# Optimization experiments

Hardware: AMD Instinct MI355X
Metric: run time of the kernel (lower is better)

The kernel has to match this reference:

```python
import jax
import jax.numpy as jnp
import numpy as np


def setup_inputs() -> dict:
    key = jax.random.key(0)
    k1, k2 = jax.random.split(key)
    B, C, H, W = 2, 256, 64, 128  # 1/8-res RAFT features of a 512x1024 image
    fmap1 = jax.random.normal(k1, (B, C, H, W), dtype=jnp.float32)
    fmap2 = jax.random.normal(k2, (B, C, H, W), dtype=jnp.float32)
    return {"fmap1": fmap1, "fmap2": fmap2, "k": 32}


def reference(fmap1, fmap2, k):
    B, C, H, W = fmap1.shape
    N = H * W
    f1 = fmap1.reshape(B, C, N)
    f2 = fmap2.reshape(B, C, N)

    # --- KNN (FAISS inner-product search), indices are non-differentiable ---
    scores = jnp.einsum('bcn,bcm->bnm', jax.lax.stop_gradient(f1),
                        jax.lax.stop_gradient(f2))  # [B, N1, N2]
    _, idx = jax.lax.top_k(scores, k)               # [B, N1, k]
    idx = jnp.transpose(idx, (0, 2, 1))             # [B, k, N1]

    # --- gather top-k target features: gathered[b,c,j,n] = f2[b,c,idx[b,j,n]] ---
    gathered = jax.vmap(lambda f, i: f[:, i])(f2, idx)  # [B, C, k, N1]

    # --- sparse correlation ---
    corr_sp = jnp.einsum('bcn,bckn->bkn', f1, gathered) / jnp.sqrt(jnp.float32(C))

    # --- coordinate grids (y-first), relative displacement ---
    ys, xs = jnp.meshgrid(jnp.arange(H, dtype=jnp.float32),
                          jnp.arange(W, dtype=jnp.float32), indexing='ij')
    coords = jnp.stack([ys.ravel(), xs.ravel()])          # [2, N], y first
    coords0 = jnp.broadcast_to(coords[None, :, None, :], (B, 2, k, N))
    coords1 = jnp.transpose(coords[:, idx], (1, 0, 2, 3))  # [B, 2, k, N]
    coords1 = coords1 - coords0                            # relative offsets

    batch_index = jnp.broadcast_to(
        jnp.arange(B, dtype=jnp.float32).reshape(B, 1, 1, 1), (B, 1, k, N))

    return corr_sp, coords0, coords1, batch_index
```

## Files before the change

### kernel.cpp

```cpp
#include <hip/hip_runtime.h>
#include <hip/hip_bf16.h>

#define B_  2
#define C_  256
#define H_  64
#define W_  128
#define N_  (H_ * W_)
#define K_  32
#define Q_  16
#define CK2 36
#define TN  32
#define TM  32
#define NHT 64
#define RR  16

typedef short  short8  __attribute__((ext_vector_type(8)));
typedef short  short4v __attribute__((ext_vector_type(4)));
typedef float  floatx4 __attribute__((ext_vector_type(4)));

__device__ __forceinline__ unsigned umin_(unsigned a, unsigned b) { return a < b ? a : b; }
__device__ __forceinline__ unsigned umax_(unsigned a, unsigned b) { return a > b ? a : b; }
__device__ __forceinline__ ushort f2bf(float v) {
    __hip_bfloat16 h = __float2bfloat16(v);
    ushort u; __builtin_memcpy(&u, &h, 2); return u;
}
__device__ __forceinline__ unsigned med3u(unsigned a, unsigned b, unsigned c) {
    unsigned d;
    asm("v_med3_u32 %0, %1, %2, %3" : "=v"(d) : "v"(a), "v"(b), "v"(c));
    return d;
}

__device__ __forceinline__ unsigned packkey(float v, int m) {
    const float vc = v > 0.0f ? v : 0.0f;
    unsigned b; __builtin_memcpy(&b, &vc, 4);
    return (b & 0xFFFFE000u) | (unsigned)m;
}

__device__ __forceinline__ void qinsert(unsigned (&q)[Q_], unsigned k) {
#pragma unroll
    for (int i = Q_ - 1; i > 0; --i)
        q[i] = med3u(q[i - 1], k, q[i]);
    q[0] = umax_(q[0], k);
}

#define CSWAP(a, b) { const unsigned _mx = umax_(a, b); \
                      const unsigned _mn = umin_(a, b); (a) = _mx; (b) = _mn; }

__device__ __forceinline__ void bar_lgkm() {
    asm volatile("s_waitcnt lgkmcnt(0)" ::: "memory");
    __builtin_amdgcn_sched_barrier(0);
    __builtin_amdgcn_s_barrier();
    __builtin_amdgcn_sched_barrier(0);
}

__global__ void raft_prep_kernel(const float* __restrict__ f1,
                                 const float* __restrict__ f2,
                                 float* __restrict__ f1Tf,
                                 ushort* __restrict__ f2T,
                                 float* __restrict__ f2Tf) {
    __shared__ float tile[32][33];
    const int nt = blockIdx.x;
    const int ct = blockIdx.y;
    const int z  = blockIdx.z;
    const int b  = z >> 1;
    const float* __restrict__ src = (z & 1) ? f2 : f1;
    const int tid = threadIdx.x;

    {
        const int cl = tid >> 3;
        const int nx = tid & 7;
        const float4 v = *(const float4*)(
            src + ((size_t)b * C_ + (ct * 32 + cl)) * N_ + (nt * 32 + nx * 4));
        tile[cl][nx * 4 + 0] = v.x;
        tile[cl][nx * 4 + 1] = v.y;
        tile[cl][nx * 4 + 2] = v.z;
        tile[cl][nx * 4 + 3] = v.w;
    }
    __syncthreads();
    {
        const int nl = tid >> 3;
        const int c4 = (tid & 7) * 4;
        float4 v;
        v.x = tile[c4 + 0][nl];
        v.y = tile[c4 + 1][nl];
        v.z = tile[c4 + 2][nl];
        v.w = tile[c4 + 3][nl];
        const size_t o = ((size_t)b * N_ + (nt * 32 + nl)) * C_ + (ct * 32 + c4);
        if (z & 1) {
            *(float4*)(f2Tf + o) = v;
            short4v h;
            h[0] = (short)f2bf(v.x); h[1] = (short)f2bf(v.y);
            h[2] = (short)f2bf(v.z); h[3] = (short)f2bf(v.w);
            *(short4v*)(f2T + o) = h;
        } else {
            *(float4*)(f1Tf + o) = v;
        }
    }
}

__launch_bounds__(512, 4)
__global__ void raft_stage1_kernel(const float* __restrict__ f1Tf,
                                   const ushort* __restrict__ f2T,
                                   ushort* __restrict__ cand) {
    __shared__ __align__(16) ushort Bt[4][TM * 256];

    const int bid0 = blockIdx.x;
    const int bid  = ((bid0 & 7) << 6) | (bid0 >> 3);
    const int b    = bid >> 8;
    const int nt0  = (bid & 255) * TN;
    const int tid  = threadIdx.x;
    const int w    = tid >> 6;
    const int s    = w & 1;
    const int h    = w >> 1;
    const int lane = tid & 63;
    const int p    = lane & 15;
    const int q4   = lane >> 4;
    const int nrow = nt0 + s * 16 + p;
    const int mbase = h * (N_ / 4);
    const int lt   = tid & 127;

    short8 af[8];
    {
        const float* __restrict__ arow = f1Tf + ((size_t)b * N_ + nrow) * C_;
        #pragma unroll
        for (int ks = 0; ks < 8; ++ks) {
            const float4 x = *(const float4*)(arow + ks * 32 + q4 * 8);
            const float4 y = *(const float4*)(arow + ks * 32 + q4 * 8 + 4);
            short8 t;
            t[0] = (short)f2bf(x.x); t[1] = (short)f2bf(x.y);
            t[2] = (short)f2bf(x.z); t[3] = (short)f2bf(x.w);
            t[4] = (short)f2bf(y.x); t[5] = (short)f2bf(y.y);
            t[6] = (short)f2bf(y.z); t[7] = (short)f2bf(y.w);
            af[ks] = t;
        }
    }

    unsigned q[Q_];
    #pragma unroll
    for (int i = 0; i < Q_; ++i) q[i] = 0u;

    const ushort* __restrict__ Bb = f2T + (size_t)b * N_ * C_ + (size_t)mbase * C_;

    short8 stg[8];
    #pragma unroll
    for (int i = 0; i < 8; ++i) {
        const int idx = lt + 128 * i;
        const int r   = idx >> 5;
        const int c8  = idx & 31;
        stg[i] = *(const short8*)(Bb + (size_t)r * C_ + c8 * 8);
    }

    for (int mt = 0; mt < NHT; ++mt) {
        {
            ushort* __restrict__ dst = Bt[h];
            #pragma unroll
            for (int i = 0; i < 8; ++i) {
                const int idx = lt + 128 * i;
                const int r   = idx >> 5;
                const int c8  = idx & 31;
                *(short8*)(&dst[(r * 32 + (c8 ^ (r & 7))) * 8]) = stg[i];
            }
        }

        if (mt < NHT - 1) {
            const ushort* __restrict__ src = Bb + (size_t)(mt + 1) * TM * C_;
            #pragma unroll
            for (int i = 0; i < 8; ++i) {
                const int idx = lt + 128 * i;
                const int r   = idx >> 5;
                const int c8  = idx & 31;
                stg[i] = *(const short8*)(src + (size_t)r * C_ + c8 * 8);
            }
        }
        bar_lgkm();

        const ushort* __restrict__ cur = Bt[h];
        floatx4 acc[2];
        #pragma unroll
        for (int f = 0; f < 2; ++f) acc[f] = (floatx4){0.f, 0.f, 0.f, 0.f};
        #pragma unroll
        for (int ks = 0; ks < 8; ++ks) {
            #pragma unroll
            for (int f = 0; f < 2; ++f) {
                const short8 bm = *(const short8*)(
                    &cur[((f * 16 + p) * 32 + ((ks * 4 + q4) ^ (p & 7))) * 8]);
                acc[f] = __builtin_amdgcn_mfma_f32_16x16x32_bf16(bm, af[ks], acc[f], 0, 0, 0);
            }
        }

        const int m0 = mbase + mt * TM;
        #pragma unroll
        for (int f = 0; f < 2; ++f) {
            const int mb = m0 + f * 16 + q4 * 4;
            unsigned k0 = packkey(acc[f][0], mb + 0);
            unsigned k1 = packkey(acc[f][1], mb + 1);
            unsigned k2 = packkey(acc[f][2], mb + 2);
            unsigned k3 = packkey(acc[f][3], mb + 3);
            CSWAP(k0, k1); CSWAP(k2, k3); CSWAP(k0, k2); CSWAP(k1, k3); CSWAP(k1, k2);
            qinsert(q, k0);
            if (__any(k1 > q[Q_ - 1])) {
                qinsert(q, k1);
                if (__any(k2 > q[Q_ - 1])) {
                    qinsert(q, k2);
                    if (__any(k3 > q[Q_ - 1])) qinsert(q, k3);
                }
            }
        }
        bar_lgkm();
    }

    unsigned* __restrict__ mg = (unsigned*)&Bt[0][0];
    const int rowl = s * 16 + p;
    const int qi   = h * 4 + q4;
    #pragma unroll
    for (int t = 0; t < Q_; ++t)
        mg[(qi * Q_ + t) * 33 + rowl] = q[t];
    __syncthreads();

    unsigned* __restrict__ ms = mg + 8448;
    if (tid < 128) {
        const int r = tid >> 2, g = tid & 3;
        const unsigned* __restrict__ Lb = &mg[(g * 4) * Q_ * 33];
        unsigned* __restrict__ O = &ms[(g * CK2) * 33 + r];
        int i0 = 0, i1 = 0, i2 = 0, i3 = 0;
        for (int t = 0; t < CK2; ++t) {
            const unsigned a0 = (i0 < Q_) ? Lb[(0 * Q_ + i0) * 33 + r] : 0u;
            const unsigned a1 = (i1 < Q_) ? Lb[(1 * Q_ + i1) * 33 + r] : 0u;
            const unsigned a2 = (i2 < Q_) ? Lb[(2 * Q_ + i2) * 33 + r] : 0u;
            const unsigned a3 = (i3 < Q_) ? Lb[(3 * Q_ + i3) * 33 + r] : 0u;
            const unsigned m01 = umax_(a0, a1), m23 = umax_(a2, a3);
            const unsigned mx  = umax_(m01, m23);
            O[t * 33] = mx;
            i0 += (a0 == mx);
            i1 += (a0 != mx) & (a1 == mx);
            i2 += (a0 != mx) & (a1 != mx) & (a2 == mx);
            i3 += (a0 != mx) & (a1 != mx) & (a2 != mx) & (a3 == mx);
        }
    }
    __syncthreads();

    if (tid < 32) {
        int i0 = 0, i1 = 0, i2 = 0, i3 = 0;
        ushort* __restrict__ myc = cand + ((size_t)(b * N_ + nt0 + tid)) * CK2;
        for (int t = 0; t < CK2; ++t) {
            const unsigned a0 = ms[(0 * CK2 + i0) * 33 + tid];
            const unsigned a1 = ms[(1 * CK2 + i1) * 33 + tid];
            const unsigned a2 = ms[(2 * CK2 + i2) * 33 + tid];
            const unsigned a3 = ms[(3 * CK2 + i3) * 33 + tid];
            const unsigned m01 = umax_(a0, a1), m23 = umax_(a2, a3);
            const unsigned mx  = umax_(m01, m23);
            myc[t] = (ushort)(mx & 0x1FFFu);
            i0 += (a0 == mx);
            i1 += (a0 != mx) & (a1 == mx);
            i2 += (a0 != mx) & (a1 != mx) & (a2 == mx);
            i3 += (a0 != mx) & (a1 != mx) & (a2 != mx) & (a3 == mx);
        }
    }
}

__launch_bounds__(576)
__global__ void raft_rerank_kernel(const float* __restrict__ f1Tf,
                                   const float* __restrict__ f2Tf,
                                   const ushort* __restrict__ cand,
                                   float* __restrict__ out) {
    __shared__ float  aS[RR][C_];
    __shared__ float  cs[RR][CK2];
    __shared__ ushort cmS[RR][CK2];
    const int bid0 = blockIdx.x;
    const int bid  = ((bid0 & 7) << 7) | (bid0 >> 3);
    const int row0 = bid * RR;
    const int tid  = threadIdx.x;
    const int r    = tid / CK2;
    const int c    = tid - r * CK2;

    for (int sidx = tid; sidx < RR * (C_ / 4); sidx += RR * CK2) {
        const int rr = sidx >> 6, s4 = sidx & 63;
        const int rg = row0 + rr;
        const int bb = rg >> 13, nn = rg & (N_ - 1);
        *(float4*)(&aS[rr][s4 * 4]) =
            *(const float4*)(f1Tf + ((size_t)bb * N_ + nn) * C_ + s4 * 4);
    }
    cmS[r][c] = cand[(size_t)(row0 + r) * CK2 + c];
    __syncthreads();

    {
        const int rg = row0 + r;
        const int bb = rg >> 13;
        const int m  = cmS[r][c];
        const float* __restrict__ bRow = f2Tf + ((size_t)bb * N_ + m) * C_;
        float acc = 0.0f;
        for (int c4 = 0; c4 < C_; c4 += 4) {
            const float4 b4 = *(const float4*)(bRow + c4);
            acc = fmaf(aS[r][c4 + 0], b4.x, acc);
            acc = fmaf(aS[r][c4 + 1], b4.y, acc);
            acc = fmaf(aS[r][c4 + 2], b4.z, acc);
            acc = fmaf(aS[r][c4 + 3], b4.w, acc);
        }
        cs[r][c] = acc;
    }
    __syncthreads();

    const int rg = row0 + r;
    const int bb = rg >> 13;
    const int n  = rg & (N_ - 1);
    const int y0 = n >> 7, x0 = n & 127;
    {
        const float v = cs[r][c];
        const int m = cmS[r][c];
        int rank = 0;
        for (int j = 0; j < CK2; ++j) {
            const float vj = cs[r][j];
            rank += (vj > v) || ((vj == v) && (cmS[r][j] < m));
        }
        if (rank < K_) {
            const size_t posn = (size_t)rank * N_ + n;
            out[(size_t)bb * (K_ * N_) + posn] = v * 0.0625f;
            const size_t c1b = (size_t)1572864 + (size_t)bb * 2 * K_ * N_;
            out[c1b + posn]                     = (float)((m >> 7) - y0);
            out[c1b + (size_t)(K_ * N_) + posn] = (float)((m & 127) - x0);
        }
    }
    if (c < K_) {
        const size_t posn = (size_t)c * N_ + n;
        const size_t c0b = (size_t)524288 + (size_t)bb * 2 * K_ * N_;
        out[c0b + posn]                     = (float)y0;
        out[c0b + (size_t)(K_ * N_) + posn] = (float)x0;
        out[(size_t)2621440 + (size_t)bb * (K_ * N_) + posn] = (float)bb;
    }
}

extern "C" void kernel_launch(void* const* d_in, const int* in_sizes, int n_in,
                              void* d_out, int out_size, void* d_ws, size_t ws_size,
                              hipStream_t stream) {
    const float* f1 = (const float*)d_in[0];
    const float* f2 = (const float*)d_in[1];

    float*  f1Tf = (float*)d_ws;
    float*  f2Tf = f1Tf + (size_t)B_ * N_ * C_;
    ushort* f2T  = (ushort*)(f2Tf + (size_t)B_ * N_ * C_);
    ushort* cand = f2T + (size_t)B_ * N_ * C_;

    raft_prep_kernel<<<dim3(N_ / 32, C_ / 32, B_ * 2), dim3(256), 0, stream>>>(
        f1, f2, f1Tf, f2T, f2Tf);

    raft_stage1_kernel<<<dim3(B_ * (N_ / TN)), dim3(512), 0, stream>>>(f1Tf, f2T, cand);

    raft_rerank_kernel<<<dim3(B_ * N_ / RR), dim3(RR * CK2), 0, stream>>>(
        f1Tf, f2Tf, cand, (float*)d_out);
}
```

Measured before the change: 347.9 us.

## Load B fragments directly to registers, drop LDS staging and barriers in stage1

The stage-1 KNN kernel no longer stages f2 tiles through shared memory with per-tile barriers. Each wave now streams its own 16-row B fragments straight from global memory into registers, prefetching the next tile during the MFMA work. Each wave covers both 16-row query halves with two accumulators and two per-lane queues, and the queue depth drops from 16 to 10. The merge stage becomes an 8-way merge to match the changed split. This removes LDS writes and barrier stalls but raises register pressure (occupancy hint lowered to 2), increases global/L2 traffic with no LDS reuse, and the shallower per-lane queues risk losing true top-k candidates.

```diff
diff --git a/kernel.cpp b/kernel.cpp
--- a/kernel.cpp
+++ b/kernel.cpp
@@ -7,10 +7,10 @@
 #define W_  128
 #define N_  (H_ * W_)
 #define K_  32
-#define Q_  16
+#define Q_  10
 #define CK2 36
 #define TN  32
-#define TM  32
+#define TM  16
 #define NHT 64
 #define RR  16
 
@@ -45,13 +45,6 @@
 
 #define CSWAP(a, b) { const unsigned _mx = umax_(a, b); \
                       const unsigned _mn = umin_(a, b); (a) = _mx; (b) = _mn; }
-
-__device__ __forceinline__ void bar_lgkm() {
-    asm volatile("s_waitcnt lgkmcnt(0)" ::: "memory");
-    __builtin_amdgcn_sched_barrier(0);
-    __builtin_amdgcn_s_barrier();
-    __builtin_amdgcn_sched_barrier(0);
-}
 
 __global__ void raft_prep_kernel(const float* __restrict__ f1,
                                  const float* __restrict__ f2,
@@ -98,30 +91,27 @@
     }
 }
 
-__launch_bounds__(512, 4)
+__launch_bounds__(512, 2)
 __global__ void raft_stage1_kernel(const float* __restrict__ f1Tf,
                                    const ushort* __restrict__ f2T,
                                    ushort* __restrict__ cand) {
-    __shared__ __align__(16) ushort Bt[4][TM * 256];
+    __shared__ unsigned smem[15840];
 
     const int bid0 = blockIdx.x;
     const int bid  = ((bid0 & 7) << 6) | (bid0 >> 3);
     const int b    = bid >> 8;
     const int nt0  = (bid & 255) * TN;
     const int tid  = threadIdx.x;
-    const int w    = tid >> 6;
-    const int s    = w & 1;
-    const int h    = w >> 1;
+    const int h    = tid >> 6;
     const int lane = tid & 63;
     const int p    = lane & 15;
     const int q4   = lane >> 4;
-    const int nrow = nt0 + s * 16 + p;
-    const int mbase = h * (N_ / 4);
-    const int lt   = tid & 127;
-
-    short8 af[8];
-    {
-        const float* __restrict__ arow = f1Tf + ((size_t)b * N_ + nrow) * C_;
+
+    short8 af[2][8];
+    #pragma unroll
+    for (int ns = 0; ns < 2; ++ns) {
+        const float* __restrict__ arow =
+            f1Tf + ((size_t)b * N_ + nt0 + ns * 16 + p) * C_;
         #pragma unroll
         for (int ks = 0; ks < 8; ++ks) {
             const float4 x = *(const float4*)(arow + ks * 32 + q4 * 8);
@@ -131,110 +121,106 @@
             t[2] = (short)f2bf(x.z); t[3] = (short)f2bf(x.w);
             t[4] = (short)f2bf(y.x); t[5] = (short)f2bf(y.y);
             t[6] = (short)f2bf(y.z); t[7] = (short)f2bf(y.w);
-            af[ks] = t;
-        }
-    }
-
-    unsigned q[Q_];
+            af[ns][ks] = t;
+        }
+    }
+
+    unsigned q0[Q_], q1[Q_];
     #pragma unroll
-    for (int i = 0; i < Q_; ++i) q[i] = 0u;
-
-    const ushort* __restrict__ Bb = f2T + (size_t)b * N_ * C_ + (size_t)mbase * C_;
-
-    short8 stg[8];
+    for (int i = 0; i < Q_; ++i) { q0[i] = 0u; q1[i] = 0u; }
+
+    const ushort* __restrict__ Bl =
+        f2T + (size_t)b * N_ * C_ + (size_t)h * 1024 * C_ + p * C_ + q4 * 8;
+
+    short8 bm[8];
     #pragma unroll
-    for (int i = 0; i < 8; ++i) {
-        const int idx = lt + 128 * i;
-        const int r   = idx >> 5;
-        const int c8  = idx & 31;
-        stg[i] = *(const short8*)(Bb + (size_t)r * C_ + c8 * 8);
-    }
+    for (int ks = 0; ks < 8; ++ks)
+        bm[ks] = *(const short8*)(Bl + ks * 32);
 
     for (int mt = 0; mt < NHT; ++mt) {
-        {
-            ushort* __restrict__ dst = Bt[h];
-            #pragma unroll
-            for (int i = 0; i < 8; ++i) {
-                const int idx = lt + 128 * i;
-                const int r   = idx >> 5;
-                const int c8  = idx & 31;
-                *(short8*)(&dst[(r * 32 + (c8 ^ (r & 7))) * 8]) = stg[i];
-            }
-        }
-
-        if (mt < NHT - 1) {
-            const ushort* __restrict__ src = Bb + (size_t)(mt + 1) * TM * C_;
-            #pragma unroll
-            for (int i = 0; i < 8; ++i) {
-                const int idx = lt + 128 * i;
-                const int r   = idx >> 5;
-                const int c8  = idx & 31;
-                stg[i] = *(const short8*)(src + (size_t)r * C_ + c8 * 8);
-            }
-        }
-        bar_lgkm();
-
-        const ushort* __restrict__ cur = Bt[h];
-        floatx4 acc[2];
-        #pragma unroll
-        for (int f = 0; f < 2; ++f) acc[f] = (floatx4){0.f, 0.f, 0.f, 0.f};
+        floatx4 acc0 = (floatx4){0.f, 0.f, 0.f, 0.f};
+        floatx4 acc1 = (floatx4){0.f, 0.f, 0.f, 0.f};
         #pragma unroll
         for (int ks = 0; ks < 8; ++ks) {
+            acc0 = __builtin_amdgcn_mfma_f32_16x16x32_bf16(bm[ks], af[0][ks], acc0, 0, 0, 0);
+            acc1 = __builtin_amdgcn_mfma_f32_16x16x32_bf16(bm[ks], af[1][ks], acc1, 0, 0, 0);
+        }
+
+        if (mt < NHT - 1) {
+            const ushort* __restrict__ src = Bl + (size_t)(mt + 1) * TM * C_;
             #pragma unroll
-            for (int f = 0; f < 2; ++f) {
-                const short8 bm = *(const short8*)(
-                    &cur[((f * 16 + p) * 32 + ((ks * 4 + q4) ^ (p & 7))) * 8]);
-                acc[f] = __builtin_amdgcn_mfma_f32_16x16x32_bf16(bm, af[ks], acc[f], 0, 0, 0);
-            }
-        }
-
-        const int m0 = mbase + mt * TM;
-        #pragma unroll
-        for (int f = 0; f < 2; ++f) {
-            const int mb = m0 + f * 16 + q4 * 4;
-            unsigned k0 = packkey(acc[f][0], mb + 0);
-            unsigned k1 = packkey(acc[f][1], mb + 1);
-            unsigned k2 = packkey(acc[f][2], mb + 2);
-            unsigned k3 = packkey(acc[f][3], mb + 3);
+            for (int ks = 0; ks < 8; ++ks)
+                bm[ks] = *(const short8*)(src + ks * 32);
+        }
+
+        const int mb = h * 1024 + mt * TM + q4 * 4;
+        {
+            unsigned k0 = packkey(acc0[0], mb + 0);
+            unsigned k1 = packkey(acc0[1], mb + 1);
+            unsigned k2 = packkey(acc0[2], mb + 2);
+            unsigned k3 = packkey(acc0[3], mb + 3);
             CSWAP(k0, k1); CSWAP(k2, k3); CSWAP(k0, k2); CSWAP(k1, k3); CSWAP(k1, k2);
-            qinsert(q, k0);
-            if (__any(k1 > q[Q_ - 1])) {
-                qinsert(q, k1);
-                if (__any(k2 > q[Q_ - 1])) {
-                    qinsert(q, k2);
-                    if (__any(k3 > q[Q_ - 1])) qinsert(q, k3);
+            qinsert(q0, k0);
+            if (__any(k1 > q0[Q_ - 1])) {
+                qinsert(q0, k1);
+                if (__any(k2 > q0[Q_ - 1])) {
+                    qinsert(q0, k2);
+                    if (__any(k3 > q0[Q_ - 1])) qinsert(q0, k3);
                 }
             }
         }
-        bar_lgkm();
-    }
-
-    unsigned* __restrict__ mg = (unsigned*)&Bt[0][0];
-    const int rowl = s * 16 + p;
-    const int qi   = h * 4 + q4;
+        {
+            unsigned k0 = packkey(acc1[0], mb + 0);
+            unsigned k1 = packkey(acc1[1], mb + 1);
+            unsigned k2 = packkey(acc1[2], mb + 2);
+            unsigned k3 = packkey(acc1[3], mb + 3);
+            CSWAP(k0, k1); CSWAP(k2, k3); CSWAP(k0, k2); CSWAP(k1, k3); CSWAP(k1, k2);
+            qinsert(q1, k0);
+            if (__any(k1 > q1[Q_ - 1])) {
+                qinsert(q1, k1);
+                if (__any(k2 > q1[Q_ - 1])) {
+                    qinsert(q1, k2);
+                    if (__any(k3 > q1[Q_ - 1])) qinsert(q1, k3);
+                }
+            }
+        }
+    }
+
+    const int qi = h * 4 + q4;
     #pragma unroll
-    for (int t = 0; t < Q_; ++t)
-        mg[(qi * Q_ + t) * 33 + rowl] = q[t];
-    __syncthreads();
-
-    unsigned* __restrict__ ms = mg + 8448;
+    for (int t = 0; t < Q_; ++t) {
+        smem[(qi * Q_ + t) * 33 + p]      = q0[t];
+        smem[(qi * Q_ + t) * 33 + 16 + p] = q1[t];
+    }
+    __syncthreads();
+
+    unsigned* __restrict__ ms = smem + 10560;
     if (tid < 128) {
         const int r = tid >> 2, g = tid & 3;
-        const unsigned* __restrict__ Lb = &mg[(g * 4) * Q_ * 33];
-        unsigned* __restrict__ O = &ms[(g * CK2) * 33 + r];
-        int i0 = 0, i1 = 0, i2 = 0, i3 = 0;
+        const int lb = g * 8;
+        int i0 = 0, i1 = 0, i2 = 0, i3 = 0, i4 = 0, i5 = 0, i6 = 0, i7 = 0;
         for (int t = 0; t < CK2; ++t) {
-            const unsigned a0 = (i0 < Q_) ? Lb[(0 * Q_ + i0) * 33 + r] : 0u;
-            const unsigned a1 = (i1 < Q_) ? Lb[(1 * Q_ + i1) * 33 + r] : 0u;
-            const unsigned a2 = (i2 < Q_) ? Lb[(2 * Q_ + i2) * 33 + r] : 0u;
-            const unsigned a3 = (i3 < Q_) ? Lb[(3 * Q_ + i3) * 33 + r] : 0u;
-            const unsigned m01 = umax_(a0, a1), m23 = umax_(a2, a3);
-            const unsigned mx  = umax_(m01, m23);
-            O[t * 33] = mx;
-            i0 += (a0 == mx);
-            i1 += (a0 != mx) & (a1 == mx);
-            i2 += (a0 != mx) & (a1 != mx) & (a2 == mx);
-            i3 += (a0 != mx) & (a1 != mx) & (a2 != mx) & (a3 == mx);
+            const unsigned a0 = (i0 < Q_) ? smem[((lb + 0) * Q_ + i0) * 33 + r] : 0u;
+            const unsigned a1 = (i1 < Q_) ? smem[((lb + 1) * Q_ + i1) * 33 + r] : 0u;
+            const unsigned a2 = (i2 < Q_) ? smem[((lb + 2) * Q_ + i2) * 33 + r] : 0u;
+            const unsigned a3 = (i3 < Q_) ? smem[((lb + 3) * Q_ + i3) * 33 + r] : 0u;
+            const unsigned a4 = (i4 < Q_) ? smem[((lb + 4) * Q_ + i4) * 33 + r] : 0u;
+            const unsigned a5 = (i5 < Q_) ? smem[((lb + 5) * Q_ + i5) * 33 + r] : 0u;
+            const unsigned a6 = (i6 < Q_) ? smem[((lb + 6) * Q_ + i6) * 33 + r] : 0u;
+            const unsigned a7 = (i7 < Q_) ? smem[((lb + 7) * Q_ + i7) * 33 + r] : 0u;
+            const unsigned mx = umax_(umax_(umax_(a0, a1), umax_(a2, a3)),
+                                      umax_(umax_(a4, a5), umax_(a6, a7)));
+            ms[(g * CK2 + t) * 33 + r] = mx;
+            const bool e0 = (a0 == mx);
+            const bool e1 = !e0 && (a1 == mx);
+            const bool e2 = !e0 && !e1 && (a2 == mx);
+            const bool e3 = !e0 && !e1 && !e2 && (a3 == mx);
+            const bool e4 = !e0 && !e1 && !e2 && !e3 && (a4 == mx);
+            const bool e5 = !e0 && !e1 && !e2 && !e3 && !e4 && (a5 == mx);
+            const bool e6 = !e0 && !e1 && !e2 && !e3 && !e4 && !e5 && (a6 == mx);
+            const bool e7 = !e0 && !e1 && !e2 && !e3 && !e4 && !e5 && !e6 && (a7 == mx);
+            i0 += e0; i1 += e1; i2 += e2; i3 += e3;
+            i4 += e4; i5 += e5; i6 += e6; i7 += e7;
         }
     }
     __syncthreads();
```

New measurement: 456.4 us. 1.31x slower.
